# Kernel optimization log

Hardware: AMD Instinct MI355X
Metric: run time of the kernel (lower is better)

Reference implementation:

```python
import jax, jax.numpy as jnp
import numpy as np

S, D, H, F = 4096, 1024, 16, 4096
DH = D // H  # 64
EPS = 1e-6


def _layer_norm(x, scale, bias):
    mu = jnp.mean(x, axis=-1, keepdims=True)
    var = jnp.mean(jnp.square(x - mu), axis=-1, keepdims=True)
    return (x - mu) * jax.lax.rsqrt(var + EPS) * scale + bias


def setup_inputs() -> dict:
    key = jax.random.key(0)
    ks = jax.random.split(key, 12)
    s = 0.02
    return {
        "x": jax.random.normal(ks[0], (S, D), jnp.float32),
        "Wq": jax.random.normal(ks[1], (D, H, DH), jnp.float32) * s,
        "bq": jnp.zeros((H, DH), jnp.float32),
        "Wk": jax.random.normal(ks[2], (D, H, DH), jnp.float32) * s,
        "bk": jnp.zeros((H, DH), jnp.float32),
        "Wv": jax.random.normal(ks[3], (D, H, DH), jnp.float32) * s,
        "bv": jnp.zeros((H, DH), jnp.float32),
        "Wo": jax.random.normal(ks[4], (H, DH, D), jnp.float32) * s,
        "bo": jnp.zeros((D,), jnp.float32),
        "ln1_scale": jnp.ones((D,), jnp.float32),
        "ln1_bias": jnp.zeros((D,), jnp.float32),
        "ln2_scale": jnp.ones((D,), jnp.float32),
        "ln2_bias": jnp.zeros((D,), jnp.float32),
        "W1": jax.random.normal(ks[5], (D, F), jnp.float32) * s,
        "b1": jnp.zeros((F,), jnp.float32),
        "W2": jax.random.normal(ks[6], (F, D), jnp.float32) * s,
        "b2": jnp.zeros((D,), jnp.float32),
    }


def reference(x, Wq, bq, Wk, bk, Wv, bv, Wo, bo,
              ln1_scale, ln1_bias, ln2_scale, ln2_bias,
              W1, b1, W2, b2):
    # --- attention block (pre-LN, no mask, no dropout, no RoPE) ---
    y = _layer_norm(x, ln1_scale, ln1_bias)            # [S, D]
    q = jnp.einsum("sd,dhk->shk", y, Wq) + bq          # [S, H, DH]
    k = jnp.einsum("sd,dhk->shk", y, Wk) + bk
    v = jnp.einsum("sd,dhk->shk", y, Wv) + bv
    scale = jnp.float32(1.0 / np.sqrt(DH))
    scores = jnp.einsum("qhd,khd->hqk", q * scale, k)  # [H, S, S]
    w = jax.nn.softmax(scores, axis=-1)
    ctx = jnp.einsum("hqk,khd->qhd", w, v)             # [S, H, DH]
    attn_out = jnp.einsum("qhd,hdo->qo", ctx, Wo) + bo  # [S, D]
    x = x + attn_out
    # --- FFN block ---
    y = _layer_norm(x, ln2_scale, ln2_bias)
    y = jax.nn.gelu(y @ W1 + b1, approximate=False)
    y = y @ W2 + b2
    return x + y
```

## Files before the change

### kernel.cpp

```cpp
#include <hip/hip_runtime.h>
#include <cstdint>
#include <cstddef>


typedef __attribute__((ext_vector_type(8))) __bf16 bf16x8;
typedef __attribute__((ext_vector_type(4))) float f32x4;
typedef __attribute__((ext_vector_type(2))) float f32x2;
typedef __attribute__((ext_vector_type(16))) float f32x16;
typedef __attribute__((ext_vector_type(4))) unsigned int u32x4;

__device__ inline unsigned short f2bf(float f) {
  unsigned int u = __float_as_uint(f);
  u += 0x7fffu + ((u >> 16) & 1u);
  return (unsigned short)(u >> 16);
}

__device__ inline void gload_lds16(const unsigned short* g, unsigned short* l) {
  __builtin_amdgcn_global_load_lds(
      (const __attribute__((address_space(1))) void*)g,
      (__attribute__((address_space(3))) void*)l, 16, 0, 0);
}

__global__ __launch_bounds__(256) void transpose_cvt(const float* __restrict__ in,
                                                     unsigned short* __restrict__ out,
                                                     int K, int N) {
  __shared__ float t[32][33];
  int nb = blockIdx.x * 32, kb = blockIdx.y * 32;
  int tx = threadIdx.x & 31, ty = threadIdx.x >> 5;
#pragma unroll
  for (int i = 0; i < 32; i += 8)
    t[ty + i][tx] = in[(size_t)(kb + ty + i) * N + nb + tx];
  __syncthreads();
#pragma unroll
  for (int i = 0; i < 32; i += 8)
    out[(size_t)(nb + ty + i) * K + kb + tx] = f2bf(t[tx][ty + i]);
}

__global__ __launch_bounds__(256) void concat3(const float* __restrict__ a,
                                               const float* __restrict__ b,
                                               const float* __restrict__ c,
                                               float* __restrict__ out) {
  int i = blockIdx.x * 256 + threadIdx.x;
  float v = (i < 1024) ? a[i] : (i < 2048 ? b[i - 1024] : c[i - 2048]);
  out[i] = v;
}

__global__ __launch_bounds__(256) void ln_kernel(const float* __restrict__ x,
                                                 const float* __restrict__ gamma,
                                                 const float* __restrict__ beta,
                                                 unsigned short* __restrict__ y) {
  int row = blockIdx.x, tid = threadIdx.x;
  const float4 v = ((const float4*)(x + (size_t)row * 1024))[tid];
  float s = v.x + v.y + v.z + v.w;
#pragma unroll
  for (int off = 1; off < 64; off <<= 1) s += __shfl_xor(s, off);
  __shared__ float red1[4], red2[4];
  int wave = tid >> 6;
  if ((tid & 63) == 0) red1[wave] = s;
  __syncthreads();
  float mu = (red1[0] + red1[1] + red1[2] + red1[3]) * (1.0f / 1024.0f);
  float dx = v.x - mu, dy = v.y - mu, dz = v.z - mu, dw = v.w - mu;
  float s2 = dx * dx + dy * dy + dz * dz + dw * dw;
#pragma unroll
  for (int off = 1; off < 64; off <<= 1) s2 += __shfl_xor(s2, off);
  if ((tid & 63) == 0) red2[wave] = s2;
  __syncthreads();
  float var = (red2[0] + red2[1] + red2[2] + red2[3]) * (1.0f / 1024.0f);
  float inv = rsqrtf(var + 1e-6f);
  int c = tid * 4;
  ushort4 o;
  o.x = f2bf(dx * inv * gamma[c + 0] + beta[c + 0]);
  o.y = f2bf(dy * inv * gamma[c + 1] + beta[c + 1]);
  o.z = f2bf(dz * inv * gamma[c + 2] + beta[c + 2]);
  o.w = f2bf(dw * inv * gamma[c + 3] + beta[c + 3]);
  ((ushort4*)(y + (size_t)row * 1024))[tid] = o;
}

template <int TM, bool GELU, bool RES, bool OUTBF, bool SCALEQ>
__global__ __launch_bounds__(256) void gemm_bt(const unsigned short* __restrict__ A,
                                               const unsigned short* __restrict__ BT,
                                               const float* __restrict__ bias,
                                               const float* __restrict__ res,
                                               void* __restrict__ out,
                                               int M, int N, int K) {
  constexpr int AI = TM / 32;
  __shared__ unsigned short As[TM * 32];
  __shared__ unsigned short Bs[128 * 32];
  int bm = blockIdx.x, bn = blockIdx.y;
  int tid = threadIdx.x;
  int wave = tid >> 6, lane = tid & 63, quad = lane >> 4, l16 = lane & 15;
  int wrow = (wave >> 1) * (16 * AI), wcol = (wave & 1) * 64;
  f32x4 zero = {0.f, 0.f, 0.f, 0.f};
  f32x4 acc[AI][4];
#pragma unroll
  for (int i = 0; i < AI; i++)
#pragma unroll
    for (int j = 0; j < 4; j++) acc[i][j] = zero;

  const int srow = tid >> 2;
  const int scol = (tid & 3) * 8;
  const unsigned short* aG0 = A + (size_t)(bm * TM + srow) * K + scol;
  const unsigned short* aG1 = A + (size_t)(bm * TM + 64 + srow) * K + scol;
  const unsigned short* bG0 = BT + (size_t)(bn * 128 + srow) * K + scol;
  const unsigned short* bG1 = BT + (size_t)(bn * 128 + 64 + srow) * K + scol;
  unsigned short* aL0 = As + (size_t)tid * 8;
  unsigned short* aL1 = As + (size_t)(256 + tid) * 8;
  unsigned short* bL0 = Bs + (size_t)tid * 8;
  unsigned short* bL1 = Bs + (size_t)(256 + tid) * 8;

  for (int k0 = 0; k0 < K; k0 += 32) {
    __syncthreads();
    gload_lds16(aG0 + k0, aL0);
    if (TM == 128) gload_lds16(aG1 + k0, aL1);
    gload_lds16(bG0 + k0, bL0);
    gload_lds16(bG1 + k0, bL1);
    __syncthreads();
    bf16x8 af[AI], bfr[4];
#pragma unroll
    for (int i = 0; i < AI; i++) af[i] = *(const bf16x8*)&As[(wrow + i * 16 + l16) * 32 + quad * 8];
#pragma unroll
    for (int j = 0; j < 4; j++) bfr[j] = *(const bf16x8*)&Bs[(wcol + j * 16 + l16) * 32 + quad * 8];
#pragma unroll
    for (int i = 0; i < AI; i++)
#pragma unroll
      for (int j = 0; j < 4; j++)
        acc[i][j] = __builtin_amdgcn_mfma_f32_16x16x32_bf16(af[i], bfr[j], acc[i][j], 0, 0, 0);
  }

#pragma unroll
  for (int i = 0; i < AI; i++) {
    int row = bm * TM + wrow + i * 16 + quad * 4;
#pragma unroll
    for (int j = 0; j < 4; j++) {
      int col = bn * 128 + wcol + j * 16 + l16;
      float bv = bias[col];
      float qs = (SCALEQ && col < 1024) ? 0.18033688f : 1.0f;
#pragma unroll
      for (int r = 0; r < 4; r++) {
        float v = (acc[i][j][r] + bv) * qs;
        if (GELU) v = 0.5f * v * (1.0f + erff(v * 0.70710678118654752440f));
        if (RES) v += res[(size_t)(row + r) * N + col];
        if (OUTBF)
          ((unsigned short*)out)[(size_t)(row + r) * N + col] = f2bf(v);
        else
          ((float*)out)[(size_t)(row + r) * N + col] = v;
      }
    }
  }
}

__global__ __launch_bounds__(256) void prep_kv(const unsigned short* __restrict__ qkv,
                                               unsigned short* __restrict__ Kp,
                                               unsigned short* __restrict__ Vp) {
  __shared__ unsigned short Vt[64 * 64];
  int t = blockIdx.x, h = blockIdx.y;
  int tid = threadIdx.x;
  const int r2 = tid >> 3, c0 = (tid & 7) * 8;
  size_t tb = ((size_t)h * 64 + t) * 4096;
  {
    const unsigned short* kp = qkv + (size_t)(t * 64 + r2) * 3072 + 1024 + h * 64 + c0;
    uint4 k0 = *(const uint4*)kp;
    uint4 k1 = *(const uint4*)(kp + (size_t)32 * 3072);
    int c = c0 >> 3;
    *(uint4*)(Kp + tb + c * 512 + r2 * 8) = k0;
    *(uint4*)(Kp + tb + c * 512 + (r2 + 32) * 8) = k1;
  }
  {
    const unsigned short* vp = qkv + (size_t)(t * 64 + 2 * r2) * 3072 + 2048 + h * 64 + c0;
    uint4 v0 = *(const uint4*)vp;
    uint4 v1 = *(const uint4*)(vp + 3072);
    const unsigned short* p0 = (const unsigned short*)&v0;
    const unsigned short* p1 = (const unsigned short*)&v1;
#pragma unroll
    for (int dd = 0; dd < 8; dd++) {
      unsigned int pk = (unsigned int)p0[dd] | ((unsigned int)p1[dd] << 16);
      *(unsigned int*)&Vt[(c0 + dd) * 64 + 2 * r2] = pk;
    }
  }
  __syncthreads();
#pragma unroll
  for (int u0 = 0; u0 < 2; u0++) {
    int u = tid + u0 * 256;
    *(uint4*)(Vp + tb + u * 8) = *(const uint4*)&Vt[(u & 63) * 64 + (u >> 6) * 8];
  }
}

__global__ __launch_bounds__(256, 3) void attn_kernel(const unsigned short* __restrict__ qkv,
                                                      const unsigned short* __restrict__ Kp,
                                                      const unsigned short* __restrict__ Vp,
                                                      unsigned short* __restrict__ ctx) {
  __shared__ float comb[2 * 32 * 64];
  __shared__ float lpart[4 * 32];
  int qt = blockIdx.x, h = blockIdx.y;
  int tid = threadIdx.x;
  int w = tid >> 6, lane = tid & 63;
  int l31 = lane & 31, hi = lane >> 5;
  int qsub = w & 1, kvh = w >> 1;

  bf16x8 qf[4];
  {
    const unsigned short* qp = qkv + (size_t)(qt * 64 + qsub * 32 + l31) * 3072 + h * 64 + hi * 8;
#pragma unroll
    for (int kk = 0; kk < 4; kk++) qf[kk] = *(const bf16x8*)(qp + kk * 16);
  }

  const size_t hb = (size_t)h * 64 * 4096;
  const unsigned short* kB = Kp + hb + hi * 512 + (kvh * 32 + l31) * 8;
  const unsigned short* vB = Vp + hb + (kvh * 4 + hi) * 512 + l31 * 8;

  f32x16 accO0, accO1;
  f32x2 lp2 = {0.f, 0.f};
#pragma unroll
  for (int r = 0; r < 16; r++) { accO0[r] = 0.f; accO1[r] = 0.f; }

  bf16x8 kf[4];
#pragma unroll
  for (int kk = 0; kk < 4; kk++) kf[kk] = *(const bf16x8*)(kB + kk * 1024);

  for (int t = 0; t < 64; t++) {
    const unsigned short* vt = vB + (size_t)t * 4096;
    bf16x8 vA0 = *(const bf16x8*)(vt);
    bf16x8 vA1 = *(const bf16x8*)(vt + 1024);
    bf16x8 vB0 = *(const bf16x8*)(vt + 256);
    bf16x8 vB1 = *(const bf16x8*)(vt + 1024 + 256);

    f32x16 accS;
#pragma unroll
    for (int r = 0; r < 16; r++) accS[r] = 0.f;
#pragma unroll
    for (int kk = 0; kk < 4; kk++)
      accS = __builtin_amdgcn_mfma_f32_32x32x16_bf16(kf[kk], qf[kk], accS, 0, 0, 0);

    if (t < 63) {
      const unsigned short* kt = kB + (size_t)(t + 1) * 4096;
#pragma unroll
      for (int kk = 0; kk < 4; kk++) kf[kk] = *(const bf16x8*)(kt + kk * 1024);
    }

    unsigned int pd[8];
#pragma unroll
    for (int i = 0; i < 8; i++) {
      float a = __builtin_amdgcn_exp2f(accS[2 * i]);
      float b = __builtin_amdgcn_exp2f(accS[2 * i + 1]);
      f32x2 ab = {a, b};
      lp2 += ab;
      pd[i] = __builtin_amdgcn_perm(__float_as_uint(b), __float_as_uint(a), 0x07060302);
    }
    asm("v_permlane32_swap_b32 %0, %1" : "+v"(pd[0]), "+v"(pd[2]));
    asm("v_permlane32_swap_b32 %0, %1" : "+v"(pd[1]), "+v"(pd[3]));
    asm("v_permlane32_swap_b32 %0, %1" : "+v"(pd[4]), "+v"(pd[6]));
    asm("v_permlane32_swap_b32 %0, %1" : "+v"(pd[5]), "+v"(pd[7]));
    u32x4 f0 = {pd[0], pd[1], pd[2], pd[3]};
    u32x4 f1 = {pd[4], pd[5], pd[6], pd[7]};
    bf16x8 pa0 = __builtin_bit_cast(bf16x8, f0);
    bf16x8 pa1 = __builtin_bit_cast(bf16x8, f1);

    accO0 = __builtin_amdgcn_mfma_f32_32x32x16_bf16(pa0, vA0, accO0, 0, 0, 0);
    accO1 = __builtin_amdgcn_mfma_f32_32x32x16_bf16(pa0, vB0, accO1, 0, 0, 0);
    accO0 = __builtin_amdgcn_mfma_f32_32x32x16_bf16(pa1, vA1, accO0, 0, 0, 0);
    accO1 = __builtin_amdgcn_mfma_f32_32x32x16_bf16(pa1, vB1, accO1, 0, 0, 0);
  }

  float lp = lp2.x + lp2.y;
  lp += __shfl_xor(lp, 32);
  if (hi == 0) lpart[(kvh * 2 + qsub) * 32 + l31] = lp;
  if (kvh == 1) {
#pragma unroll
    for (int r = 0; r < 16; r++) {
      int q = (r & 3) + 8 * (r >> 2) + 4 * hi;
      comb[(qsub * 32 + q) * 64 + l31] = accO0[r];
      comb[(qsub * 32 + q) * 64 + 32 + l31] = accO1[r];
    }
  }
  __syncthreads();
  if (kvh == 0) {
#pragma unroll
    for (int r = 0; r < 16; r++) {
      int q = (r & 3) + 8 * (r >> 2) + 4 * hi;
      float l = lpart[qsub * 32 + q] + lpart[(2 + qsub) * 32 + q];
      float inv = 1.0f / l;
      float v0 = (accO0[r] + comb[(qsub * 32 + q) * 64 + l31]) * inv;
      float v1 = (accO1[r] + comb[(qsub * 32 + q) * 64 + 32 + l31]) * inv;
      int row = qt * 64 + qsub * 32 + q;
      size_t o = (size_t)row * 1024 + h * 64;
      ctx[o + l31] = f2bf(v0);
      ctx[o + 32 + l31] = f2bf(v1);
    }
  }
}

extern "C" void kernel_launch(void* const* d_in, const int* in_sizes, int n_in,
                              void* d_out, int out_size, void* d_ws, size_t ws_size,
                              hipStream_t stream) {
  const float* x   = (const float*)d_in[0];
  const float* Wq  = (const float*)d_in[1];
  const float* bq  = (const float*)d_in[2];
  const float* Wk  = (const float*)d_in[3];
  const float* bk  = (const float*)d_in[4];
  const float* Wv  = (const float*)d_in[5];
  const float* bv  = (const float*)d_in[6];
  const float* Wo  = (const float*)d_in[7];
  const float* bo  = (const float*)d_in[8];
  const float* g1  = (const float*)d_in[9];
  const float* be1 = (const float*)d_in[10];
  const float* g2  = (const float*)d_in[11];
  const float* be2 = (const float*)d_in[12];
  const float* W1  = (const float*)d_in[13];
  const float* b1  = (const float*)d_in[14];
  const float* W2  = (const float*)d_in[15];
  const float* b2  = (const float*)d_in[16];
  float* out = (float*)d_out;

  char* p = (char*)d_ws;
  unsigned short* WqkvT = (unsigned short*)p; p += (size_t)3072 * 1024 * 2;
  unsigned short* WoT   = (unsigned short*)p; p += (size_t)1024 * 1024 * 2;
  unsigned short* W1T   = (unsigned short*)p; p += (size_t)4096 * 1024 * 2;
  unsigned short* W2T   = (unsigned short*)p; p += (size_t)1024 * 4096 * 2;
  float*          bqkv  = (float*)p;          p += 16384;
  unsigned short* y1    = (unsigned short*)p; p += (size_t)4096 * 1024 * 2;
  unsigned short* qkvb  = (unsigned short*)p; p += (size_t)4096 * 3072 * 2;
  unsigned short* ctxb  = (unsigned short*)p; p += (size_t)4096 * 1024 * 2;
  float*          x1    = (float*)p;          p += (size_t)4096 * 1024 * 4;
  unsigned short* Kp    = (unsigned short*)p; p += (size_t)16 * 64 * 4096 * 2;
  unsigned short* Vp    = (unsigned short*)p; p += (size_t)16 * 64 * 4096 * 2;
  unsigned short* hbuf  = qkvb;

  dim3 b256(256);
  transpose_cvt<<<dim3(32, 32), b256, 0, stream>>>(Wq, WqkvT, 1024, 1024);
  transpose_cvt<<<dim3(32, 32), b256, 0, stream>>>(Wk, WqkvT + (size_t)1024 * 1024, 1024, 1024);
  transpose_cvt<<<dim3(32, 32), b256, 0, stream>>>(Wv, WqkvT + (size_t)2048 * 1024, 1024, 1024);
  transpose_cvt<<<dim3(32, 32), b256, 0, stream>>>(Wo, WoT, 1024, 1024);
  transpose_cvt<<<dim3(128, 32), b256, 0, stream>>>(W1, W1T, 1024, 4096);
  transpose_cvt<<<dim3(32, 128), b256, 0, stream>>>(W2, W2T, 4096, 1024);
  concat3<<<12, b256, 0, stream>>>(bq, bk, bv, bqkv);

  ln_kernel<<<4096, b256, 0, stream>>>(x, g1, be1, y1);
  gemm_bt<128, false, false, true, true><<<dim3(32, 24), b256, 0, stream>>>(y1, WqkvT, bqkv, nullptr, qkvb, 4096, 3072, 1024);
  prep_kv<<<dim3(64, 16), b256, 0, stream>>>(qkvb, Kp, Vp);
  attn_kernel<<<dim3(64, 16), b256, 0, stream>>>(qkvb, Kp, Vp, ctxb);
  gemm_bt<64, false, true, false, false><<<dim3(64, 8), b256, 0, stream>>>(ctxb, WoT, bo, x, x1, 4096, 1024, 1024);
  ln_kernel<<<4096, b256, 0, stream>>>(x1, g2, be2, y1);
  gemm_bt<128, true, false, true, false><<<dim3(32, 32), b256, 0, stream>>>(y1, W1T, b1, nullptr, hbuf, 4096, 4096, 1024);
  gemm_bt<64, false, true, false, false><<<dim3(64, 8), b256, 0, stream>>>(hbuf, W2T, b2, x1, out, 4096, 1024, 4096);
}
```

Before: 445.4 us.

## Split attention KV range across four waves, each covering all 64 queries

Each of the four waves in the attention block now processes all 64 query rows (two 32-row sub-tiles) against its own quarter of the key/value sequence. Before, each wave handled 32 queries over half the keys. Every loaded K/V fragment now feeds two query sub-tiles, which halves K/V global traffic per MFMA. The cost is more accumulator registers (four 32x32 output tiles per wave) and a bigger LDS reduction buffer, 48KB plus the lpart array, to combine the partials of four waves. Both could lower occupancy at the launch bound of 3 blocks per CU.

Measured after the change: 459.6 us. +3.2%, slower.

```diff
diff --git a/kernel.cpp b/kernel.cpp
--- a/kernel.cpp
+++ b/kernel.cpp
@@ -189,103 +189,122 @@
                                                       const unsigned short* __restrict__ Kp,
                                                       const unsigned short* __restrict__ Vp,
                                                       unsigned short* __restrict__ ctx) {
-  __shared__ float comb[2 * 32 * 64];
-  __shared__ float lpart[4 * 32];
+  __shared__ float comb[3 * 64 * 64];
+  __shared__ float lpart[4 * 64];
   int qt = blockIdx.x, h = blockIdx.y;
   int tid = threadIdx.x;
   int w = tid >> 6, lane = tid & 63;
   int l31 = lane & 31, hi = lane >> 5;
-  int qsub = w & 1, kvh = w >> 1;
-
-  bf16x8 qf[4];
-  {
-    const unsigned short* qp = qkv + (size_t)(qt * 64 + qsub * 32 + l31) * 3072 + h * 64 + hi * 8;
-#pragma unroll
-    for (int kk = 0; kk < 4; kk++) qf[kk] = *(const bf16x8*)(qp + kk * 16);
-  }
-
-  const size_t hb = (size_t)h * 64 * 4096;
-  const unsigned short* kB = Kp + hb + hi * 512 + (kvh * 32 + l31) * 8;
-  const unsigned short* vB = Vp + hb + (kvh * 4 + hi) * 512 + l31 * 8;
-
-  f32x16 accO0, accO1;
-  f32x2 lp2 = {0.f, 0.f};
-#pragma unroll
-  for (int r = 0; r < 16; r++) { accO0[r] = 0.f; accO1[r] = 0.f; }
+
+  bf16x8 qf[2][4];
+#pragma unroll
+  for (int qt2 = 0; qt2 < 2; qt2++) {
+    const unsigned short* qp = qkv + (size_t)(qt * 64 + qt2 * 32 + l31) * 3072 + h * 64 + hi * 8;
+#pragma unroll
+    for (int kk = 0; kk < 4; kk++) qf[qt2][kk] = *(const bf16x8*)(qp + kk * 16);
+  }
+
+  const size_t hb = (size_t)h * 262144;
+  const unsigned short* kB = Kp + hb + (size_t)(w >> 1) * 4096 + hi * 512 + ((w & 1) * 32 + l31) * 8;
+  const unsigned short* vB = Vp + hb + (size_t)(w >> 1) * 4096 + ((w & 1) * 4 + hi) * 512 + l31 * 8;
+
+  f32x16 accO[2][2];
+  f32x2 lp2[2] = {{0.f, 0.f}, {0.f, 0.f}};
+#pragma unroll
+  for (int a = 0; a < 2; a++)
+#pragma unroll
+    for (int b = 0; b < 2; b++)
+#pragma unroll
+      for (int r = 0; r < 16; r++) accO[a][b][r] = 0.f;
 
   bf16x8 kf[4];
 #pragma unroll
   for (int kk = 0; kk < 4; kk++) kf[kk] = *(const bf16x8*)(kB + kk * 1024);
 
-  for (int t = 0; t < 64; t++) {
-    const unsigned short* vt = vB + (size_t)t * 4096;
-    bf16x8 vA0 = *(const bf16x8*)(vt);
-    bf16x8 vA1 = *(const bf16x8*)(vt + 1024);
-    bf16x8 vB0 = *(const bf16x8*)(vt + 256);
-    bf16x8 vB1 = *(const bf16x8*)(vt + 1024 + 256);
-
-    f32x16 accS;
-#pragma unroll
-    for (int r = 0; r < 16; r++) accS[r] = 0.f;
-#pragma unroll
-    for (int kk = 0; kk < 4; kk++)
-      accS = __builtin_amdgcn_mfma_f32_32x32x16_bf16(kf[kk], qf[kk], accS, 0, 0, 0);
-
-    if (t < 63) {
-      const unsigned short* kt = kB + (size_t)(t + 1) * 4096;
-#pragma unroll
-      for (int kk = 0; kk < 4; kk++) kf[kk] = *(const bf16x8*)(kt + kk * 1024);
+  for (int t = 0; t < 32; t++) {
+    const unsigned short* vt = vB + (size_t)t * 8192;
+    bf16x8 vf00 = *(const bf16x8*)(vt);
+    bf16x8 vf01 = *(const bf16x8*)(vt + 256);
+    bf16x8 vf10 = *(const bf16x8*)(vt + 1024);
+    bf16x8 vf11 = *(const bf16x8*)(vt + 1024 + 256);
+
+#pragma unroll
+    for (int qt2 = 0; qt2 < 2; qt2++) {
+      f32x16 accS;
+#pragma unroll
+      for (int r = 0; r < 16; r++) accS[r] = 0.f;
+#pragma unroll
+      for (int kk = 0; kk < 4; kk++)
+        accS = __builtin_amdgcn_mfma_f32_32x32x16_bf16(kf[kk], qf[qt2][kk], accS, 0, 0, 0);
+
+      if (qt2 == 1 && t < 31) {
+        const unsigned short* kt = kB + (size_t)(t + 1) * 8192;
+#pragma unroll
+        for (int kk = 0; kk < 4; kk++) kf[kk] = *(const bf16x8*)(kt + kk * 1024);
+      }
+
+      unsigned int pd[8];
+#pragma unroll
+      for (int i = 0; i < 8; i++) {
+        float a = __builtin_amdgcn_exp2f(accS[2 * i]);
+        float b = __builtin_amdgcn_exp2f(accS[2 * i + 1]);
+        f32x2 ab = {a, b};
+        lp2[qt2] += ab;
+        pd[i] = __builtin_amdgcn_perm(__float_as_uint(b), __float_as_uint(a), 0x07060302);
+      }
+      asm("v_permlane32_swap_b32 %0, %1" : "+v"(pd[0]), "+v"(pd[2]));
+      asm("v_permlane32_swap_b32 %0, %1" : "+v"(pd[1]), "+v"(pd[3]));
+      asm("v_permlane32_swap_b32 %0, %1" : "+v"(pd[4]), "+v"(pd[6]));
+      asm("v_permlane32_swap_b32 %0, %1" : "+v"(pd[5]), "+v"(pd[7]));
+      u32x4 f0 = {pd[0], pd[1], pd[2], pd[3]};
+      u32x4 f1 = {pd[4], pd[5], pd[6], pd[7]};
+      bf16x8 pa0 = __builtin_bit_cast(bf16x8, f0);
+      bf16x8 pa1 = __builtin_bit_cast(bf16x8, f1);
+
+      accO[qt2][0] = __builtin_amdgcn_mfma_f32_32x32x16_bf16(pa0, vf00, accO[qt2][0], 0, 0, 0);
+      accO[qt2][1] = __builtin_amdgcn_mfma_f32_32x32x16_bf16(pa0, vf01, accO[qt2][1], 0, 0, 0);
+      accO[qt2][0] = __builtin_amdgcn_mfma_f32_32x32x16_bf16(pa1, vf10, accO[qt2][0], 0, 0, 0);
+      accO[qt2][1] = __builtin_amdgcn_mfma_f32_32x32x16_bf16(pa1, vf11, accO[qt2][1], 0, 0, 0);
     }
-
-    unsigned int pd[8];
-#pragma unroll
-    for (int i = 0; i < 8; i++) {
-      float a = __builtin_amdgcn_exp2f(accS[2 * i]);
-      float b = __builtin_amdgcn_exp2f(accS[2 * i + 1]);
-      f32x2 ab = {a, b};
-      lp2 += ab;
-      pd[i] = __builtin_amdgcn_perm(__float_as_uint(b), __float_as_uint(a), 0x07060302);
-    }
-    asm("v_permlane32_swap_b32 %0, %1" : "+v"(pd[0]), "+v"(pd[2]));
-    asm("v_permlane32_swap_b32 %0, %1" : "+v"(pd[1]), "+v"(pd[3]));
-    asm("v_permlane32_swap_b32 %0, %1" : "+v"(pd[4]), "+v"(pd[6]));
-    asm("v_permlane32_swap_b32 %0, %1" : "+v"(pd[5]), "+v"(pd[7]));
-    u32x4 f0 = {pd[0], pd[1], pd[2], pd[3]};
-    u32x4 f1 = {pd[4], pd[5], pd[6], pd[7]};
-    bf16x8 pa0 = __builtin_bit_cast(bf16x8, f0);
-    bf16x8 pa1 = __builtin_bit_cast(bf16x8, f1);
-
-    accO0 = __builtin_amdgcn_mfma_f32_32x32x16_bf16(pa0, vA0, accO0, 0, 0, 0);
-    accO1 = __builtin_amdgcn_mfma_f32_32x32x16_bf16(pa0, vB0, accO1, 0, 0, 0);
-    accO0 = __builtin_amdgcn_mfma_f32_32x32x16_bf16(pa1, vA1, accO0, 0, 0, 0);
-    accO1 = __builtin_amdgcn_mfma_f32_32x32x16_bf16(pa1, vB1, accO1, 0, 0, 0);
-  }
-
-  float lp = lp2.x + lp2.y;
-  lp += __shfl_xor(lp, 32);
-  if (hi == 0) lpart[(kvh * 2 + qsub) * 32 + l31] = lp;
-  if (kvh == 1) {
-#pragma unroll
-    for (int r = 0; r < 16; r++) {
-      int q = (r & 3) + 8 * (r >> 2) + 4 * hi;
-      comb[(qsub * 32 + q) * 64 + l31] = accO0[r];
-      comb[(qsub * 32 + q) * 64 + 32 + l31] = accO1[r];
-    }
-  }
-  __syncthreads();
-  if (kvh == 0) {
-#pragma unroll
-    for (int r = 0; r < 16; r++) {
-      int q = (r & 3) + 8 * (r >> 2) + 4 * hi;
-      float l = lpart[qsub * 32 + q] + lpart[(2 + qsub) * 32 + q];
-      float inv = 1.0f / l;
-      float v0 = (accO0[r] + comb[(qsub * 32 + q) * 64 + l31]) * inv;
-      float v1 = (accO1[r] + comb[(qsub * 32 + q) * 64 + 32 + l31]) * inv;
-      int row = qt * 64 + qsub * 32 + q;
-      size_t o = (size_t)row * 1024 + h * 64;
-      ctx[o + l31] = f2bf(v0);
-      ctx[o + 32 + l31] = f2bf(v1);
-    }
+  }
+
+  float lp0 = lp2[0].x + lp2[0].y;
+  float lp1 = lp2[1].x + lp2[1].y;
+  lp0 += __shfl_xor(lp0, 32);
+  lp1 += __shfl_xor(lp1, 32);
+  if (hi == 0) {
+    lpart[w * 64 + l31] = lp0;
+    lpart[w * 64 + 32 + l31] = lp1;
+  }
+  if (w > 0) {
+    float* cw = comb + (w - 1) * 4096;
+#pragma unroll
+    for (int qt2 = 0; qt2 < 2; qt2++)
+#pragma unroll
+      for (int r = 0; r < 16; r++) {
+        int q = qt2 * 32 + (r & 3) + 8 * (r >> 2) + 4 * hi;
+        cw[q * 64 + l31] = accO[qt2][0][r];
+        cw[q * 64 + 32 + l31] = accO[qt2][1][r];
+      }
+  }
+  __syncthreads();
+  if (w == 0) {
+#pragma unroll
+    for (int qt2 = 0; qt2 < 2; qt2++)
+#pragma unroll
+      for (int r = 0; r < 16; r++) {
+        int q = qt2 * 32 + (r & 3) + 8 * (r >> 2) + 4 * hi;
+        float l = lpart[q] + lpart[64 + q] + lpart[128 + q] + lpart[192 + q];
+        float inv = 1.0f / l;
+        float v0 = accO[qt2][0][r] + comb[q * 64 + l31] + comb[4096 + q * 64 + l31] +
+                   comb[8192 + q * 64 + l31];
+        float v1 = accO[qt2][1][r] + comb[q * 64 + 32 + l31] + comb[4096 + q * 64 + 32 + l31] +
+                   comb[8192 + q * 64 + 32 + l31];
+        int row = qt * 64 + q;
+        size_t o = (size_t)row * 1024 + h * 64;
+        ctx[o + l31] = f2bf(v0 * inv);
+        ctx[o + 32 + l31] = f2bf(v1 * inv);
+      }
   }
 }
 
```

## Split attention KV range four ways per 32-query block, doubling grid

Applied to the files above, without the earlier changes.

The attention kernel now gives each block 32 query rows instead of 64. All four waves work on the same queries, each covering a quarter of the key/value sequence with a 32-step loop. Partial outputs and row sums from three waves are combined through enlarged shared memory by wave 0, and the grid doubles to 128x16 blocks with launch bounds raised to 4 blocks per CU. This adds parallelism and occupancy, at the cost of reading K/V twice as often overall and a larger cross-wave reduction.

Result: no change. 450.4 us (+1.1%).

```diff
diff --git a/kernel.cpp b/kernel.cpp
--- a/kernel.cpp
+++ b/kernel.cpp
@@ -185,28 +185,27 @@
   }
 }
 
-__global__ __launch_bounds__(256, 3) void attn_kernel(const unsigned short* __restrict__ qkv,
+__global__ __launch_bounds__(256, 4) void attn_kernel(const unsigned short* __restrict__ qkv,
                                                       const unsigned short* __restrict__ Kp,
                                                       const unsigned short* __restrict__ Vp,
                                                       unsigned short* __restrict__ ctx) {
-  __shared__ float comb[2 * 32 * 64];
+  __shared__ float comb[3 * 32 * 64];
   __shared__ float lpart[4 * 32];
   int qt = blockIdx.x, h = blockIdx.y;
   int tid = threadIdx.x;
   int w = tid >> 6, lane = tid & 63;
   int l31 = lane & 31, hi = lane >> 5;
-  int qsub = w & 1, kvh = w >> 1;
 
   bf16x8 qf[4];
   {
-    const unsigned short* qp = qkv + (size_t)(qt * 64 + qsub * 32 + l31) * 3072 + h * 64 + hi * 8;
+    const unsigned short* qp = qkv + (size_t)(qt * 32 + l31) * 3072 + h * 64 + hi * 8;
 #pragma unroll
     for (int kk = 0; kk < 4; kk++) qf[kk] = *(const bf16x8*)(qp + kk * 16);
   }
 
-  const size_t hb = (size_t)h * 64 * 4096;
-  const unsigned short* kB = Kp + hb + hi * 512 + (kvh * 32 + l31) * 8;
-  const unsigned short* vB = Vp + hb + (kvh * 4 + hi) * 512 + l31 * 8;
+  const size_t hb = (size_t)h * 262144;
+  const unsigned short* kB = Kp + hb + (size_t)(w >> 1) * 4096 + hi * 512 + ((w & 1) * 32 + l31) * 8;
+  const unsigned short* vB = Vp + hb + (size_t)(w >> 1) * 4096 + ((w & 1) * 4 + hi) * 512 + l31 * 8;
 
   f32x16 accO0, accO1;
   f32x2 lp2 = {0.f, 0.f};
@@ -217,12 +216,12 @@
 #pragma unroll
   for (int kk = 0; kk < 4; kk++) kf[kk] = *(const bf16x8*)(kB + kk * 1024);
 
-  for (int t = 0; t < 64; t++) {
-    const unsigned short* vt = vB + (size_t)t * 4096;
-    bf16x8 vA0 = *(const bf16x8*)(vt);
-    bf16x8 vA1 = *(const bf16x8*)(vt + 1024);
-    bf16x8 vB0 = *(const bf16x8*)(vt + 256);
-    bf16x8 vB1 = *(const bf16x8*)(vt + 1024 + 256);
+  for (int t = 0; t < 32; t++) {
+    const unsigned short* vt = vB + (size_t)t * 8192;
+    bf16x8 vf00 = *(const bf16x8*)(vt);
+    bf16x8 vf01 = *(const bf16x8*)(vt + 256);
+    bf16x8 vf10 = *(const bf16x8*)(vt + 1024);
+    bf16x8 vf11 = *(const bf16x8*)(vt + 1024 + 256);
 
     f32x16 accS;
 #pragma unroll
@@ -231,8 +230,8 @@
     for (int kk = 0; kk < 4; kk++)
       accS = __builtin_amdgcn_mfma_f32_32x32x16_bf16(kf[kk], qf[kk], accS, 0, 0, 0);
 
-    if (t < 63) {
-      const unsigned short* kt = kB + (size_t)(t + 1) * 4096;
+    if (t < 31) {
+      const unsigned short* kt = kB + (size_t)(t + 1) * 8192;
 #pragma unroll
       for (int kk = 0; kk < 4; kk++) kf[kk] = *(const bf16x8*)(kt + kk * 1024);
     }
@@ -255,36 +254,39 @@
     bf16x8 pa0 = __builtin_bit_cast(bf16x8, f0);
     bf16x8 pa1 = __builtin_bit_cast(bf16x8, f1);
 
-    accO0 = __builtin_amdgcn_mfma_f32_32x32x16_bf16(pa0, vA0, accO0, 0, 0, 0);
-    accO1 = __builtin_amdgcn_mfma_f32_32x32x16_bf16(pa0, vB0, accO1, 0, 0, 0);
-    accO0 = __builtin_amdgcn_mfma_f32_32x32x16_bf16(pa1, vA1, accO0, 0, 0, 0);
-    accO1 = __builtin_amdgcn_mfma_f32_32x32x16_bf16(pa1, vB1, accO1, 0, 0, 0);
+    accO0 = __builtin_amdgcn_mfma_f32_32x32x16_bf16(pa0, vf00, accO0, 0, 0, 0);
+    accO1 = __builtin_amdgcn_mfma_f32_32x32x16_bf16(pa0, vf01, accO1, 0, 0, 0);
+    accO0 = __builtin_amdgcn_mfma_f32_32x32x16_bf16(pa1, vf10, accO0, 0, 0, 0);
+    accO1 = __builtin_amdgcn_mfma_f32_32x32x16_bf16(pa1, vf11, accO1, 0, 0, 0);
   }
 
   float lp = lp2.x + lp2.y;
   lp += __shfl_xor(lp, 32);
-  if (hi == 0) lpart[(kvh * 2 + qsub) * 32 + l31] = lp;
-  if (kvh == 1) {
+  if (hi == 0) lpart[w * 32 + l31] = lp;
+  if (w > 0) {
+    float* cw = comb + (w - 1) * 2048;
 #pragma unroll
     for (int r = 0; r < 16; r++) {
       int q = (r & 3) + 8 * (r >> 2) + 4 * hi;
-      comb[(qsub * 32 + q) * 64 + l31] = accO0[r];
-      comb[(qsub * 32 + q) * 64 + 32 + l31] = accO1[r];
-    }
-  }
-  __syncthreads();
-  if (kvh == 0) {
+      cw[q * 64 + l31] = accO0[r];
+      cw[q * 64 + 32 + l31] = accO1[r];
+    }
+  }
+  __syncthreads();
+  if (w == 0) {
 #pragma unroll
     for (int r = 0; r < 16; r++) {
       int q = (r & 3) + 8 * (r >> 2) + 4 * hi;
-      float l = lpart[qsub * 32 + q] + lpart[(2 + qsub) * 32 + q];
+      float l = lpart[q] + lpart[32 + q] + lpart[64 + q] + lpart[96 + q];
       float inv = 1.0f / l;
-      float v0 = (accO0[r] + comb[(qsub * 32 + q) * 64 + l31]) * inv;
-      float v1 = (accO1[r] + comb[(qsub * 32 + q) * 64 + 32 + l31]) * inv;
-      int row = qt * 64 + qsub * 32 + q;
+      float v0 = accO0[r] + comb[q * 64 + l31] + comb[2048 + q * 64 + l31] +
+                 comb[4096 + q * 64 + l31];
+      float v1 = accO1[r] + comb[q * 64 + 32 + l31] + comb[2048 + q * 64 + 32 + l31] +
+                 comb[4096 + q * 64 + 32 + l31];
+      int row = qt * 32 + q;
       size_t o = (size_t)row * 1024 + h * 64;
-      ctx[o + l31] = f2bf(v0);
-      ctx[o + 32 + l31] = f2bf(v1);
+      ctx[o + l31] = f2bf(v0 * inv);
+      ctx[o + 32 + l31] = f2bf(v1 * inv);
     }
   }
 }
@@ -337,7 +339,7 @@
   ln_kernel<<<4096, b256, 0, stream>>>(x, g1, be1, y1);
   gemm_bt<128, false, false, true, true><<<dim3(32, 24), b256, 0, stream>>>(y1, WqkvT, bqkv, nullptr, qkvb, 4096, 3072, 1024);
   prep_kv<<<dim3(64, 16), b256, 0, stream>>>(qkvb, Kp, Vp);
-  attn_kernel<<<dim3(64, 16), b256, 0, stream>>>(qkvb, Kp, Vp, ctxb);
+  attn_kernel<<<dim3(128, 16), b256, 0, stream>>>(qkvb, Kp, Vp, ctxb);
   gemm_bt<64, false, true, false, false><<<dim3(64, 8), b256, 0, stream>>>(ctxb, WoT, bo, x, x1, 4096, 1024, 1024);
   ln_kernel<<<4096, b256, 0, stream>>>(x1, g2, be2, y1);
   gemm_bt<128, true, false, true, false><<<dim3(32, 32), b256, 0, stream>>>(y1, W1T, b1, nullptr, hbuf, 4096, 4096, 1024);
```
